# Performance work log

Measured on AMD Instinct MI355X. Metric: run time of the kernel, lower is better.

The kernel has to match this reference:

```python
import jax, jax.numpy as jnp
import numpy as np

B, N = 64, 1024


def setup_inputs() -> dict:
    key = jax.random.key(0)
    attns = jax.random.uniform(key, (B, N, N), dtype=jnp.float32)
    return {"attns": attns}


def _diag_means(a):
    # a: [B, n, n]. wave[b, d] = mean_i a[b, i, i+d] over the anti-diagonal offset d = j - i >= 0.
    n = a.shape[-1]
    idx = jnp.arange(n)
    off = idx[None, :] - idx[:, None]            # [n, n], j - i
    mask = off >= 0                              # upper triangle incl. diagonal
    seg = jnp.where(mask, off, 0).reshape(-1)    # lower-tri values are zeroed, so seg 0 is safe
    vals = jnp.where(mask, a, 0.0).reshape(a.shape[0], -1)  # [B, n*n]
    sums = jax.vmap(lambda v: jax.ops.segment_sum(v, seg, num_segments=n))(vals)  # [B, n]
    counts = (n - idx).astype(a.dtype)           # n - d elements on offset-d diagonal
    return sums / counts


def reference(attns):
    waves = _diag_means(attns)                       # [B, N]
    # torch.fft on (real, 0) pairs + L2 norm over (re, im) == FFT magnitude
    spec = jnp.abs(jnp.fft.fft(waves, axis=-1))      # [B, N]
    n = waves.shape[-1]
    sel = spec[:, 1:1 + n // 2]                      # frequencies 1 .. n/2 (exclusive of DC)
    judgement = 1.0 - jnp.max(sel, axis=-1) / jnp.sum(sel, axis=-1)  # peak-ratio per sample
    return jnp.mean(judgement)                       # scalar, mean over batch
```

## Files before the change

kernel.cpp:

```cpp
#include <hip/hip_runtime.h>

#define NN 1024
#define BB 64
#define CHUNKS 32
#define KS 8

__global__ __launch_bounds__(256) void diag_partial(const float* __restrict__ attns,
                                                    float* __restrict__ partial) {
    __shared__ float lds[4][1032];
    const int t = blockIdx.x;
    const int b = blockIdx.y;
    const int tid = threadIdx.x;
    const int w = tid >> 6, lane = tid & 63;

    float4 acc0 = make_float4(0.f, 0.f, 0.f, 0.f);
    float4 acc1 = acc0, acc2 = acc0, acc3 = acc0;

    const float* base = attns + (size_t)b * NN * NN;

#define ROWPAIR(k, fT, fB, nvT, nvB)                                          \
    const int jbT##k = 16 * t + 4 * (k);                                      \
    const int nvT = 256 - 4 * t - (k);                                        \
    const float4* fT = (const float4*)(base + (size_t)(jbT##k + w) * NN + jbT##k); \
    const int jbB##k = 1008 - 16 * t + 4 * (k);                               \
    const int nvB = 4 + 4 * t - (k);                                          \
    const float4* fB = (const float4*)(base + (size_t)(jbB##k + w) * NN + jbB##k);

    ROWPAIR(0, fT0, fB0, nvT0, nvB0)
    ROWPAIR(1, fT1, fB1, nvT1, nvB1)
    ROWPAIR(2, fT2, fB2, nvT2, nvB2)
    ROWPAIR(3, fT3, fB3, nvT3, nvB3)
#undef ROWPAIR

#define LOADP(g, fT, fB, nvT, nvB)                                            \
    float4 xa##g = fT[lane];                                                  \
    float4 xb##g = fT[lane + 64];                                             \
    float4 xc##g = fT[lane + 128 < nvT - 1 ? lane + 128 : nvT - 1];           \
    float4 xd##g = fT[lane + 192 < nvT - 1 ? lane + 192 : nvT - 1];           \
    float4 ya##g = fB[lane < nvB - 1 ? lane : nvB - 1];                       \
    float4 yb##g = fB[lane + 64 < nvB - 1 ? lane + 64 : nvB - 1];

#define CONSP(g, nvT, nvB)                                                    \
    {                                                                         \
        const bool ok2 = lane + 128 < nvT, ok3 = lane + 192 < nvT;            \
        const bool p0 = lane < nvB, p1 = lane + 64 < nvB;                     \
        xc##g.x = ok2 ? xc##g.x : 0.f; xc##g.y = ok2 ? xc##g.y : 0.f;         \
        xc##g.z = ok2 ? xc##g.z : 0.f; xc##g.w = ok2 ? xc##g.w : 0.f;         \
        xd##g.x = ok3 ? xd##g.x : 0.f; xd##g.y = ok3 ? xd##g.y : 0.f;         \
        xd##g.z = ok3 ? xd##g.z : 0.f; xd##g.w = ok3 ? xd##g.w : 0.f;         \
        ya##g.x = p0 ? ya##g.x : 0.f; ya##g.y = p0 ? ya##g.y : 0.f;           \
        ya##g.z = p0 ? ya##g.z : 0.f; ya##g.w = p0 ? ya##g.w : 0.f;           \
        yb##g.x = p1 ? yb##g.x : 0.f; yb##g.y = p1 ? yb##g.y : 0.f;           \
        yb##g.z = p1 ? yb##g.z : 0.f; yb##g.w = p1 ? yb##g.w : 0.f;           \
        if (lane == 0) {                                                      \
            if (w > 0) { xa##g.x = 0.f; ya##g.x = 0.f; }                      \
            if (w > 1) { xa##g.y = 0.f; ya##g.y = 0.f; }                      \
            if (w > 2) { xa##g.z = 0.f; ya##g.z = 0.f; }                      \
        }                                                                     \
        acc0.x += xa##g.x + ya##g.x; acc0.y += xa##g.y + ya##g.y;             \
        acc0.z += xa##g.z + ya##g.z; acc0.w += xa##g.w + ya##g.w;             \
        acc1.x += xb##g.x + yb##g.x; acc1.y += xb##g.y + yb##g.y;             \
        acc1.z += xb##g.z + yb##g.z; acc1.w += xb##g.w + yb##g.w;             \
        acc2.x += xc##g.x; acc2.y += xc##g.y;                                 \
        acc2.z += xc##g.z; acc2.w += xc##g.w;                                 \
        acc3.x += xd##g.x; acc3.y += xd##g.y;                                 \
        acc3.z += xd##g.z; acc3.w += xd##g.w;                                 \
    }

    LOADP(0, fT0, fB0, nvT0, nvB0)
    LOADP(1, fT1, fB1, nvT1, nvB1)
    LOADP(2, fT2, fB2, nvT2, nvB2)
    CONSP(0, nvT0, nvB0)
    LOADP(3, fT3, fB3, nvT3, nvB3)
    CONSP(1, nvT1, nvB1)
    CONSP(2, nvT2, nvB2)
    CONSP(3, nvT3, nvB3)
#undef LOADP
#undef CONSP

    float4* lrow = (float4*)lds[w];
    lrow[lane]       = acc0;
    lrow[lane + 64]  = acc1;
    lrow[lane + 128] = acc2;
    lrow[lane + 192] = acc3;
    if (tid < 32) lds[tid >> 3][1024 + (tid & 7)] = 0.f;
    __syncthreads();

    float* outp = partial + ((size_t)b * CHUNKS + t) * NN;
    {
        const int d0 = tid * 4;
        float4 o;
        o.x = (lds[0][d0]     + lds[1][d0 + 1]) + (lds[2][d0 + 2] + lds[3][d0 + 3]);
        o.y = (lds[0][d0 + 1] + lds[1][d0 + 2]) + (lds[2][d0 + 3] + lds[3][d0 + 4]);
        o.z = (lds[0][d0 + 2] + lds[1][d0 + 3]) + (lds[2][d0 + 4] + lds[3][d0 + 5]);
        o.w = (lds[0][d0 + 3] + lds[1][d0 + 4]) + (lds[2][d0 + 5] + lds[3][d0 + 6]);
        ((float4*)outp)[tid] = o;
    }
}

__global__ __launch_bounds__(256) void reduce_waves(const float* __restrict__ partial,
                                                    float* __restrict__ wpm) {
    __shared__ float slo_s[256], shi_s[256];
    const int blk = blockIdx.x;
    const int b = blk >> 3;
    const int dq = blk & 7;
    const int tid = threadIdx.x;
    const int d = dq * 64 + (tid & 63);
    const int cq = tid >> 6;
    const float* pb = partial + (size_t)b * CHUNKS * NN;
    float slo = 0.f, shi = 0.f;
#pragma unroll
    for (int j = 0; j < 8; ++j) {
        const int c = cq * 8 + j;
        slo += pb[c * NN + d];
        shi += pb[c * NN + d + 512];
    }
    slo_s[tid] = slo; shi_s[tid] = shi;
    __syncthreads();
    if (tid < 64) {
        const float l = (slo_s[tid] + slo_s[tid + 64]) + (slo_s[tid + 128] + slo_s[tid + 192]);
        const float h = (shi_s[tid] + shi_s[tid + 64]) + (shi_s[tid + 128] + shi_s[tid + 192]);
        const float wlo = l / (float)(NN - d);
        const float whi = h / (float)(512 - d);
        wpm[(size_t)b * NN + d]       = wlo + whi;
        wpm[(size_t)b * NN + 512 + d] = wlo - whi;
    }
}

__global__ __launch_bounds__(512) void dft_part(const float* __restrict__ wpm,
                                                float* __restrict__ kparts) {
    __shared__ float wp[512], wm[512];
    __shared__ float2 tw[NN];
    __shared__ float redmax[8], redsum[8];
    const int ks = blockIdx.x & (KS - 1);
    const int b = blockIdx.x >> 3;
    const int tid = threadIdx.x;
    const float C = 6.283185307179586f / 1024.0f;

    {
        const float* src = wpm + (size_t)b * NN;
        wp[tid & 511] = src[tid & 511];
        wm[tid & 511] = src[512 + (tid & 511)];
        float s0, c0, s1, c1;
        __sincosf((float)tid * C, &s0, &c0);
        __sincosf((float)(tid + 512) * C, &s1, &c1);
        tw[tid]       = make_float2(c0, -s0);
        tw[tid + 512] = make_float2(c1, -s1);
    }
    __syncthreads();

    const int k = 1 + ks * 64 + (tid >> 3);
    const int dp = tid & 7;
    const float* wsel = (k & 1) ? wm : wp;
    const int kstep = (k << 3) & (NN - 1);

    float re = 0.f, im = 0.f;
    int t = (k * dp) & (NN - 1);
#pragma unroll 8
    for (int it = 0; it < 64; ++it) {
        const float2 c = tw[t];
        const float wv = wsel[dp + 8 * it];
        re = fmaf(wv, c.x, re);
        im = fmaf(wv, c.y, im);
        t = (t + kstep) & (NN - 1);
    }
    re += __shfl_xor(re, 1, 64); re += __shfl_xor(re, 2, 64); re += __shfl_xor(re, 4, 64);
    im += __shfl_xor(im, 1, 64); im += __shfl_xor(im, 2, 64); im += __shfl_xor(im, 4, 64);
    const float spec = sqrtf(re * re + im * im);

    float mx = spec;
    float sm = (dp == 0) ? spec : 0.f;
    for (int off = 8; off < 64; off <<= 1) {
        mx = fmaxf(mx, __shfl_xor(mx, off, 64));
        sm += __shfl_xor(sm, off, 64);
    }
    const int wid = tid >> 6, lane = tid & 63;
    if (lane == 0) { redmax[wid] = mx; redsum[wid] = sm; }
    __syncthreads();
    if (tid == 0) {
        float M = redmax[0], S = redsum[0];
        for (int i = 1; i < 8; ++i) { M = fmaxf(M, redmax[i]); S += redsum[i]; }
        kparts[((size_t)b * KS + ks) * 2 + 0] = M;
        kparts[((size_t)b * KS + ks) * 2 + 1] = S;
    }
}

__global__ __launch_bounds__(64) void finalize(const float* __restrict__ kparts,
                                               float* __restrict__ out) {
    const int lane = threadIdx.x;
    float M = 0.f, S = 0.f;
#pragma unroll
    for (int s = 0; s < KS; ++s) {
        M = fmaxf(M, kparts[((size_t)lane * KS + s) * 2 + 0]);
        S += kparts[((size_t)lane * KS + s) * 2 + 1];
    }
    float j = 1.0f - M / S;
    for (int off = 32; off; off >>= 1) j += __shfl_xor(j, off, 64);
    if (lane == 0) out[0] = j * (1.0f / 64.0f);
}

extern "C" void kernel_launch(void* const* d_in, const int* in_sizes, int n_in,
                              void* d_out, int out_size, void* d_ws, size_t ws_size,
                              hipStream_t stream) {
    const float* attns = (const float*)d_in[0];
    float* out = (float*)d_out;

    float* partial = (float*)d_ws;
    float* wpm     = partial + (size_t)BB * CHUNKS * NN;
    float* kparts  = wpm + (size_t)BB * NN;

    diag_partial<<<dim3(CHUNKS, BB), 256, 0, stream>>>(attns, partial);
    reduce_waves<<<BB * 8, 256, 0, stream>>>(partial, wpm);
    dft_part<<<BB * KS, 512, 0, stream>>>(wpm, kparts);
    finalize<<<1, 64, 0, stream>>>(kparts, out);
}
```

Before: 39.99 us.

## Halve diagonal chunks and fold finalize into DFT via last-block atomic ticket

Each diag_partial block now handles eight row-groups instead of four, halving the number of chunks. That halves the partial buffer the reduce kernel has to read and write. The separate finalize launch is removed: each DFT block takes an atomic ticket, and the last block does the batch mean. This saves a kernel launch and some intermediate traffic, but it costs less parallelism in the first kernel and depends on the counter being reset inside diag_partial.

```diff
diff --git a/kernel.cpp b/kernel.cpp
--- a/kernel.cpp
+++ b/kernel.cpp
@@ -2,48 +2,45 @@
 
 #define NN 1024
 #define BB 64
-#define CHUNKS 32
+#define CHUNKS 16
 #define KS 8
 
 __global__ __launch_bounds__(256) void diag_partial(const float* __restrict__ attns,
-                                                    float* __restrict__ partial) {
+                                                    float* __restrict__ partial,
+                                                    unsigned* __restrict__ counter) {
     __shared__ float lds[4][1032];
     const int t = blockIdx.x;
     const int b = blockIdx.y;
     const int tid = threadIdx.x;
     const int w = tid >> 6, lane = tid & 63;
 
+    if (t == 0 && b == 0 && tid == 0) *counter = 0u;
+
     float4 acc0 = make_float4(0.f, 0.f, 0.f, 0.f);
     float4 acc1 = acc0, acc2 = acc0, acc3 = acc0;
 
     const float* base = attns + (size_t)b * NN * NN;
 
-#define ROWPAIR(k, fT, fB, nvT, nvB)                                          \
-    const int jbT##k = 16 * t + 4 * (k);                                      \
-    const int nvT = 256 - 4 * t - (k);                                        \
-    const float4* fT = (const float4*)(base + (size_t)(jbT##k + w) * NN + jbT##k); \
-    const int jbB##k = 1008 - 16 * t + 4 * (k);                               \
-    const int nvB = 4 + 4 * t - (k);                                          \
-    const float4* fB = (const float4*)(base + (size_t)(jbB##k + w) * NN + jbB##k);
-
-    ROWPAIR(0, fT0, fB0, nvT0, nvB0)
-    ROWPAIR(1, fT1, fB1, nvT1, nvB1)
-    ROWPAIR(2, fT2, fB2, nvT2, nvB2)
-    ROWPAIR(3, fT3, fB3, nvT3, nvB3)
-#undef ROWPAIR
-
-#define LOADP(g, fT, fB, nvT, nvB)                                            \
-    float4 xa##g = fT[lane];                                                  \
-    float4 xb##g = fT[lane + 64];                                             \
-    float4 xc##g = fT[lane + 128 < nvT - 1 ? lane + 128 : nvT - 1];           \
-    float4 xd##g = fT[lane + 192 < nvT - 1 ? lane + 192 : nvT - 1];           \
-    float4 ya##g = fB[lane < nvB - 1 ? lane : nvB - 1];                       \
-    float4 yb##g = fB[lane + 64 < nvB - 1 ? lane + 64 : nvB - 1];
-
-#define CONSP(g, nvT, nvB)                                                    \
+#define ROWPAIR(g, kk)                                                        \
+    const int jbT##g = 32 * t + 4 * (kk);                                     \
+    const int nvT##g = 256 - 8 * t - (kk);                                    \
+    const float4* fT##g = (const float4*)(base + (size_t)(jbT##g + w) * NN + jbT##g); \
+    const int jbB##g = 992 - 32 * t + 4 * (kk);                               \
+    const int nvB##g = 8 + 8 * t - (kk);                                      \
+    const float4* fB##g = (const float4*)(base + (size_t)(jbB##g + w) * NN + jbB##g);
+
+#define LOADP(g)                                                              \
+    float4 xa##g = fT##g[lane];                                               \
+    float4 xb##g = fT##g[lane + 64];                                          \
+    float4 xc##g = fT##g[lane + 128 < nvT##g - 1 ? lane + 128 : nvT##g - 1];  \
+    float4 xd##g = fT##g[lane + 192 < nvT##g - 1 ? lane + 192 : nvT##g - 1];  \
+    float4 ya##g = fB##g[lane < nvB##g - 1 ? lane : nvB##g - 1];              \
+    float4 yb##g = fB##g[lane + 64 < nvB##g - 1 ? lane + 64 : nvB##g - 1];
+
+#define CONSP(g)                                                              \
     {                                                                         \
-        const bool ok2 = lane + 128 < nvT, ok3 = lane + 192 < nvT;            \
-        const bool p0 = lane < nvB, p1 = lane + 64 < nvB;                     \
+        const bool ok2 = lane + 128 < nvT##g, ok3 = lane + 192 < nvT##g;      \
+        const bool p0 = lane < nvB##g, p1 = lane + 64 < nvB##g;               \
         xc##g.x = ok2 ? xc##g.x : 0.f; xc##g.y = ok2 ? xc##g.y : 0.f;         \
         xc##g.z = ok2 ? xc##g.z : 0.f; xc##g.w = ok2 ? xc##g.w : 0.f;         \
         xd##g.x = ok3 ? xd##g.x : 0.f; xd##g.y = ok3 ? xd##g.y : 0.f;         \
@@ -67,16 +64,28 @@
         acc3.z += xd##g.z; acc3.w += xd##g.w;                                 \
     }
 
-    LOADP(0, fT0, fB0, nvT0, nvB0)
-    LOADP(1, fT1, fB1, nvT1, nvB1)
-    LOADP(2, fT2, fB2, nvT2, nvB2)
-    CONSP(0, nvT0, nvB0)
-    LOADP(3, fT3, fB3, nvT3, nvB3)
-    CONSP(1, nvT1, nvB1)
-    CONSP(2, nvT2, nvB2)
-    CONSP(3, nvT3, nvB3)
+#define HALFBODY(K0)                                                          \
+    {                                                                         \
+        ROWPAIR(0, (K0) + 0)                                                  \
+        ROWPAIR(1, (K0) + 1)                                                  \
+        ROWPAIR(2, (K0) + 2)                                                  \
+        ROWPAIR(3, (K0) + 3)                                                  \
+        LOADP(0)                                                              \
+        LOADP(1)                                                              \
+        LOADP(2)                                                              \
+        CONSP(0)                                                              \
+        LOADP(3)                                                              \
+        CONSP(1)                                                              \
+        CONSP(2)                                                              \
+        CONSP(3)                                                              \
+    }
+
+    HALFBODY(0)
+    HALFBODY(4)
+#undef ROWPAIR
 #undef LOADP
 #undef CONSP
+#undef HALFBODY
 
     float4* lrow = (float4*)lds[w];
     lrow[lane]       = acc0;
@@ -110,8 +119,8 @@
     const float* pb = partial + (size_t)b * CHUNKS * NN;
     float slo = 0.f, shi = 0.f;
 #pragma unroll
-    for (int j = 0; j < 8; ++j) {
-        const int c = cq * 8 + j;
+    for (int j = 0; j < 4; ++j) {
+        const int c = cq * 4 + j;
         slo += pb[c * NN + d];
         shi += pb[c * NN + d + 512];
     }
@@ -128,10 +137,14 @@
 }
 
 __global__ __launch_bounds__(512) void dft_part(const float* __restrict__ wpm,
-                                                float* __restrict__ kparts) {
+                                                float* __restrict__ kparts,
+                                                unsigned* __restrict__ counter,
+                                                float* __restrict__ out,
+                                                int nblocks) {
     __shared__ float wp[512], wm[512];
     __shared__ float2 tw[NN];
     __shared__ float redmax[8], redsum[8];
+    __shared__ int lastFlag;
     const int ks = blockIdx.x & (KS - 1);
     const int b = blockIdx.x >> 3;
     const int tid = threadIdx.x;
@@ -177,26 +190,33 @@
     const int wid = tid >> 6, lane = tid & 63;
     if (lane == 0) { redmax[wid] = mx; redsum[wid] = sm; }
     __syncthreads();
+
     if (tid == 0) {
         float M = redmax[0], S = redsum[0];
         for (int i = 1; i < 8; ++i) { M = fmaxf(M, redmax[i]); S += redsum[i]; }
-        kparts[((size_t)b * KS + ks) * 2 + 0] = M;
-        kparts[((size_t)b * KS + ks) * 2 + 1] = S;
-    }
-}
-
-__global__ __launch_bounds__(64) void finalize(const float* __restrict__ kparts,
-                                               float* __restrict__ out) {
-    const int lane = threadIdx.x;
-    float M = 0.f, S = 0.f;
+        __hip_atomic_store(&kparts[((size_t)b * KS + ks) * 2 + 0], M,
+                           __ATOMIC_RELAXED, __HIP_MEMORY_SCOPE_AGENT);
+        __hip_atomic_store(&kparts[((size_t)b * KS + ks) * 2 + 1], S,
+                           __ATOMIC_RELAXED, __HIP_MEMORY_SCOPE_AGENT);
+        const unsigned ticket = __hip_atomic_fetch_add(counter, 1u,
+                                   __ATOMIC_ACQ_REL, __HIP_MEMORY_SCOPE_AGENT);
+        lastFlag = (ticket == (unsigned)(nblocks - 1));
+    }
+    __syncthreads();
+
+    if (lastFlag && tid < 64) {
+        float M = 0.f, S = 0.f;
 #pragma unroll
-    for (int s = 0; s < KS; ++s) {
-        M = fmaxf(M, kparts[((size_t)lane * KS + s) * 2 + 0]);
-        S += kparts[((size_t)lane * KS + s) * 2 + 1];
-    }
-    float j = 1.0f - M / S;
-    for (int off = 32; off; off >>= 1) j += __shfl_xor(j, off, 64);
-    if (lane == 0) out[0] = j * (1.0f / 64.0f);
+        for (int s = 0; s < KS; ++s) {
+            M = fmaxf(M, __hip_atomic_load(&kparts[((size_t)tid * KS + s) * 2 + 0],
+                                           __ATOMIC_RELAXED, __HIP_MEMORY_SCOPE_AGENT));
+            S += __hip_atomic_load(&kparts[((size_t)tid * KS + s) * 2 + 1],
+                                   __ATOMIC_RELAXED, __HIP_MEMORY_SCOPE_AGENT);
+        }
+        float j = 1.0f - M / S;
+        for (int off = 32; off; off >>= 1) j += __shfl_xor(j, off, 64);
+        if (tid == 0) out[0] = j * (1.0f / 64.0f);
+    }
 }
 
 extern "C" void kernel_launch(void* const* d_in, const int* in_sizes, int n_in,
@@ -205,12 +225,13 @@
     const float* attns = (const float*)d_in[0];
     float* out = (float*)d_out;
 
-    float* partial = (float*)d_ws;
-    float* wpm     = partial + (size_t)BB * CHUNKS * NN;
-    float* kparts  = wpm + (size_t)BB * NN;
-
-    diag_partial<<<dim3(CHUNKS, BB), 256, 0, stream>>>(attns, partial);
+    float* partial    = (float*)d_ws;
+    float* wpm        = partial + (size_t)BB * CHUNKS * NN;
+    float* kparts     = wpm + (size_t)BB * NN;
+    unsigned* counter = (unsigned*)(kparts + (size_t)BB * KS * 2);
+
+    diag_partial<<<dim3(CHUNKS, BB), 256, 0, stream>>>(attns, partial, counter);
     reduce_waves<<<BB * 8, 256, 0, stream>>>(partial, wpm);
-    dft_part<<<BB * KS, 512, 0, stream>>>(wpm, kparts);
-    finalize<<<1, 64, 0, stream>>>(kparts, out);
-}
+    const int nblocks = BB * KS;
+    dft_part<<<nblocks, 512, 0, stream>>>(wpm, kparts, counter, out, nblocks);
+}
```

Measured after the change: 45.26 us. 13.2% more time.
